# Kernel optimization log

Hardware: AMD Instinct MI355X
Metric: run time of the kernel (lower is better)

## Reference

```python
import jax, jax.numpy as jnp
import numpy as np

S, B, H, D, G = 2048, 2, 16, 128, 16  # seq, batch, heads, head_dim, v-quant groups


def setup_inputs() -> dict:
    key = jax.random.key(0)
    ks = jax.random.split(key, 9)
    # int8-valued activations stored as float (torch code does .to(torch.int8))
    q = jax.random.randint(ks[0], (S, B, H, D), -128, 128).astype(jnp.float32)
    k = jax.random.randint(ks[1], (S, B, H, D), -128, 128).astype(jnp.float32)
    v = jax.random.randint(ks[2], (S, B, H, D), -128, 128).astype(jnp.float32)
    qmin = jax.random.normal(ks[3], (S, B, H, 1), jnp.float32) * 0.01
    qscale = jax.random.uniform(ks[4], (S, B, H, 1), jnp.float32, 0.005, 0.02)
    kmin = jax.random.normal(ks[5], (S, B, H, 1), jnp.float32) * 0.01
    kscale = jax.random.uniform(ks[6], (S, B, H, 1), jnp.float32, 0.005, 0.02)
    vmin = jax.random.normal(ks[7], (G, B, H, D, 1), jnp.float32) * 0.01
    vscale = jax.random.uniform(ks[8], (G, B, H, D, 1), jnp.float32, 0.005, 0.02)
    return {"query_layer": q, "key_layer": k, "value_layer": v,
            "qmin": qmin, "qscale": qscale, "kmin": kmin, "kscale": kscale,
            "vmin": vmin, "vscale": vscale, "causal": 1}


def _attention(query_layer, key_layer, value_layer, qmin, qscale, kmin, kscale, vmin, vscale, causal):
    # s b h d -> b h s d ; emulate .to(torch.int8) (values are already int8-range ints)
    q = jnp.transpose(query_layer, (1, 2, 0, 3))
    k = jnp.transpose(key_layer, (1, 2, 0, 3))
    v = jnp.transpose(value_layer, (1, 2, 0, 3))
    # per-token quant factors: s b h 1 -> b h s 1
    qm = jnp.transpose(qmin[..., 0], (1, 2, 0))[..., None]
    qs = jnp.transpose(qscale[..., 0], (1, 2, 0))[..., None]
    km = jnp.transpose(kmin[..., 0], (1, 2, 0))[..., None]
    ksc = jnp.transpose(kscale[..., 0], (1, 2, 0))[..., None]
    # attnq_qk: dequantize per-token then QK^T
    qd = q * qs + qm
    kd = k * ksc + km
    scores = jnp.einsum('bhsd,bhtd->bhst', qd, kd)
    # softmaxq: scale by 1/sqrt(128), causal mask, softmax, int8 requant of probs
    scores = scores * jnp.float32(1.0 / np.sqrt(128.0))
    s = scores.shape[-1]
    if causal:
        mask = jnp.tril(jnp.ones((s, s), dtype=bool))
        scores = jnp.where(mask, scores, jnp.float32(-1e9))
    probs = jax.nn.softmax(scores, axis=-1)
    pmin = jnp.min(probs, axis=-1, keepdims=True)
    pmax = jnp.max(probs, axis=-1, keepdims=True)
    pscale = (pmax - pmin) / 255.0 + jnp.float32(1e-12)
    quant_prob = jnp.round((probs - pmin) / pscale)  # int8-range prob codes
    # attnq_pv: dequant probs (per query token) and V (per sequence group) then PV
    pd = quant_prob * pscale + pmin
    vm = jnp.transpose(vmin[..., 0], (1, 2, 0, 3))  # b h g d
    vs = jnp.transpose(vscale[..., 0], (1, 2, 0, 3))
    gs = v.shape[2] // vm.shape[2]  # group size along sequence
    vd = v * jnp.repeat(vs, gs, axis=2) + jnp.repeat(vm, gs, axis=2)
    out = jnp.einsum('bhst,bhtd->bhsd', pd, vd)
    b, h, sq, d = out.shape
    return jnp.transpose(out, (2, 0, 1, 3)).reshape(sq, b, h * d)  # s b (h d)


def reference(query_layer, key_layer, value_layer, qmin, qscale, kmin, kscale, vmin, vscale, causal):
    return _attention(query_layer, key_layer, value_layer, qmin, qscale, kmin, kscale, vmin, vscale, causal)
```

## Files before the change

kernel.cpp:

```cpp
#include <hip/hip_runtime.h>
#include <math.h>


#define S_LEN 2048
#define BATCH 2
#define NH    16
#define HD    128
#define RSTR  4096
#define SCALE2 (0.08838834764831845f * 1.4426950408889634f)
#define EXP2F(x) __builtin_amdgcn_exp2f(x)

typedef int v4i __attribute__((ext_vector_type(4)));
#define MFMA16(a,b,c) __builtin_amdgcn_mfma_i32_16x16x64_i8((a),(b),(c),0,0,0)

#define WS_K8   0u
#define WS_V8T  (8u*1024u*1024u)
#define WS_SQ   (16u*1024u*1024u)
#define WS_SK   (WS_SQ + 256u*1024u)
#define WS_GSV  (WS_SK + 256u*1024u)
#define WS_VSUM (WS_GSV + 256u*1024u)

__global__ __launch_bounds__(256) void prep_sums(
    const float* __restrict__ Q, const float* __restrict__ K,
    signed char* __restrict__ K8, float* __restrict__ SQs, float* __restrict__ SKs)
{
    int idx = blockIdx.x*256 + threadIdx.x;
    int tensor = blockIdx.y;
    const float* src = tensor ? K : Q;
    int tau = idx >> 5, dg = idx & 31;
    float4 x = *(const float4*)(src + (size_t)tau*128 + 4*dg);
    float ssum = x.x + x.y + x.z + x.w;
    #pragma unroll
    for (int off = 16; off >= 1; off >>= 1) ssum += __shfl_xor(ssum, off);
    if (tensor) {
        int a=(int)x.x, b2=(int)x.y, c=(int)x.z, d=(int)x.w;
        ((int*)K8)[(size_t)tau*32 + dg] = (a&255)|((b2&255)<<8)|((c&255)<<16)|((d&255)<<24);
        if ((threadIdx.x & 31) == 0) SKs[tau] = ssum;
    } else {
        if ((threadIdx.x & 31) == 0) SQs[tau] = ssum;
    }
}

__device__ __forceinline__ int sbsum(unsigned p) {
    return (int)(signed char)(p) + (int)(signed char)(p>>8)
         + (int)(signed char)(p>>16) + (int)(signed char)(p>>24);
}

__global__ __launch_bounds__(256) void prep_v(
    const float* __restrict__ V, signed char* __restrict__ V8T, float* __restrict__ GSV)
{
    __shared__ int v8i[128*33];
    int tid = threadIdx.x;
    int bh = blockIdx.x & 31, ck = blockIdx.x >> 5;
    int b = bh >> 4, h = bh & 15;
    int t0 = ck * 128;
    int boff = b*2048 + h*128;
    #pragma unroll
    for (int it = 0; it < 16; ++it) {
        int idx = tid + it*256;
        int t = idx >> 5, dw = idx & 31;
        float4 x = *(const float4*)(V + (size_t)(t0+t)*RSTR + boff + 4*dw);
        int a=(int)x.x, b2=(int)x.y, c=(int)x.z, d=(int)x.w;
        v8i[t*33 + dw] = (a&255)|((b2&255)<<8)|((c&255)<<16)|((d&255)<<24);
    }
    __syncthreads();
    #pragma unroll
    for (int it = 0; it < 4; ++it) {
        int j = tid + it*256;
        int tg = j & 31, dw = j >> 5;
        unsigned r0 = (unsigned)v8i[(4*tg+0)*33 + dw];
        unsigned r1 = (unsigned)v8i[(4*tg+1)*33 + dw];
        unsigned r2 = (unsigned)v8i[(4*tg+2)*33 + dw];
        unsigned r3 = (unsigned)v8i[(4*tg+3)*33 + dw];
        unsigned x01 = __builtin_amdgcn_perm(r1, r0, 0x05010400u);
        unsigned x23 = __builtin_amdgcn_perm(r3, r2, 0x05010400u);
        unsigned y01 = __builtin_amdgcn_perm(r1, r0, 0x07030602u);
        unsigned y23 = __builtin_amdgcn_perm(r3, r2, 0x07030602u);
        unsigned p[4];
        p[0] = __builtin_amdgcn_perm(x23, x01, 0x05040100u);
        p[1] = __builtin_amdgcn_perm(x23, x01, 0x07060302u);
        p[2] = __builtin_amdgcn_perm(y23, y01, 0x05040100u);
        p[3] = __builtin_amdgcn_perm(y23, y01, 0x07060302u);
        int s[4];
        #pragma unroll
        for (int jj = 0; jj < 4; ++jj) {
            int d = 4*dw + jj;
            *(int*)(V8T + ((size_t)bh*128 + d)*2048 + t0 + 4*tg) = (int)p[jj];
            s[jj] = sbsum(p[jj]);
        }
        #pragma unroll
        for (int off = 1; off < 32; off <<= 1) {
            #pragma unroll
            for (int jj = 0; jj < 4; ++jj) s[jj] += __shfl_xor(s[jj], off);
        }
        if (tg == 0) {
            #pragma unroll
            for (int jj = 0; jj < 4; ++jj)
                GSV[((size_t)bh*16 + ck)*128 + 4*dw + jj] = (float)s[jj];
        }
    }
}

__global__ __launch_bounds__(256) void prep_vsum(
    const float* __restrict__ GSV, const float* __restrict__ VSC,
    const float* __restrict__ VMN, float* __restrict__ VSUM)
{
    int idx = blockIdx.x*256 + threadIdx.x;
    int bh = idx >> 7, d = idx & 127;
    int b = bh >> 4, h = bh & 15;
    float acc = 0.f;
    for (int g = 0; g < 16; ++g) {
        float gs = GSV[((size_t)bh*16 + g)*128 + d];
        int vi = ((g*BATCH + b)*NH + h)*HD + d;
        acc = fmaf(VSC[vi], gs, fmaf(128.0f, VMN[vi], acc));
    }
    VSUM[bh*128 + d] = acc;
}

__global__ __launch_bounds__(256, 2) void attn_main(
    const float* __restrict__ Q,
    const signed char* __restrict__ K8, const signed char* __restrict__ V8T,
    const float* __restrict__ QMN, const float* __restrict__ QSC,
    const float* __restrict__ KMN, const float* __restrict__ KSC,
    const float* __restrict__ VMN, const float* __restrict__ VSC,
    const float* __restrict__ SQs, const float* __restrict__ SKs,
    const float* __restrict__ GSV, const float* __restrict__ VSUM,
    const int* __restrict__ CAUSAL, float* __restrict__ OUT)
{
    __shared__ __align__(16) signed char q8s[64*144];
    __shared__ __align__(16) signed char k8s[128*144];
    __shared__ __align__(16) signed char v8s[128*144];
    __shared__ __align__(16) signed char pcs[64*144];
    __shared__ float rs_c1[64], rs_c2[64], rs_c3[64];
    __shared__ float rs_mx[64], rs_den[64], rs_mn[64];
    __shared__ float rs_u1[64], rs_w1[64], rs_psc[64], rs_pmn[64];
    __shared__ float ktA[128], ktB[128], ktC[128];
    __shared__ float vsA[128], vsB[128], vsC[128];

    const int tid  = threadIdx.x;
    const int w    = tid >> 6;
    const int lane = tid & 63;
    const int n    = lane & 15;
    const int quad = lane >> 4;
    const int bhi  = blockIdx.x & 31;
    const int qt   = 31 - (int)(blockIdx.x >> 5);
    const int b    = bhi >> 4, h = bhi & 15;
    const int causal = *CAUSAL;
    const int s0   = qt * 64;
    const int boff = b*2048 + h*128;
    const v4i vzero = {0,0,0,0};
    const v4i ones  = {0x01010101,0x01010101,0x01010101,0x01010101};

    #pragma unroll
    for (int it = 0; it < 8; ++it) {
        int idx = tid + it*256;
        int row = idx >> 5, d4 = (idx & 31) << 2;
        float4 x = *(const float4*)(Q + (size_t)(s0+row)*RSTR + boff + d4);
        int a=(int)x.x, b2=(int)x.y, c=(int)x.z, d=(int)x.w;
        *(int*)(q8s + row*144 + d4) = (a&255)|((b2&255)<<8)|((c&255)<<16)|((d&255)<<24);
    }
    if (tid < 64) {
        int si = (s0 + tid)*32 + bhi;
        float qs = QSC[si], qm = QMN[si];
        rs_c1[tid] = qs; rs_c2[tid] = qm;
        rs_c3[tid] = fmaf(qs, SQs[si], 128.0f*qm);
    }
    __syncthreads();

    const int kt_end = causal ? ((s0 + 63) >> 7) : 15;

    float c1r[4], c2r[4], c3r[4]; int qgr[4];
    #pragma unroll
    for (int r = 0; r < 4; ++r) {
        int qq = 16*w + 4*quad + r;
        c1r[r] = rs_c1[qq]; c2r[r] = rs_c2[qq]; c3r[r] = rs_c3[qq];
        qgr[r] = s0 + qq;
    }
    v4i a0p = *(const v4i*)(q8s + (16*w + n)*144 + 16*quad);
    v4i a1p = *(const v4i*)(q8s + (16*w + n)*144 + 64 + 16*quad);

    float m[4], l[4], mn[4];
    #pragma unroll
    for (int r = 0; r < 4; ++r) { m[r] = -INFINITY; l[r] = 0.f; mn[r] = INFINITY; }

#define P1_TILE(MASKED)                                                          \
  do {                                                                           \
    const int t0g = kt * 128;                                                    \
    __syncthreads();                                                             \
    _Pragma("unroll")                                                            \
    for (int it = 0; it < 4; ++it) {                                             \
        int idx = tid + it*256;                                                  \
        int trow = idx >> 3, doff = (idx & 7) << 4;                              \
        *(uint4*)(k8s + trow*144 + doff) =                                       \
            *(const uint4*)(K8 + ((size_t)(t0g+trow)*32 + bhi)*128 + doff);      \
    }                                                                            \
    if (tid < 128) {                                                             \
        int si = (t0g + tid)*32 + bhi;                                           \
        ktA[tid] = KSC[si]*SCALE2; ktB[tid] = KMN[si]*SCALE2; ktC[tid] = SKs[si];\
    }                                                                            \
    __syncthreads();                                                             \
    float tmax[4], sarr[8][4];                                                   \
    _Pragma("unroll")                                                            \
    for (int r = 0; r < 4; ++r) tmax[r] = -INFINITY;                             \
    _Pragma("unroll")                                                            \
    for (int tb = 0; tb < 8; ++tb) {                                             \
        v4i b0 = *(const v4i*)(k8s + (16*tb + n)*144 + 16*quad);                 \
        v4i b1 = *(const v4i*)(k8s + (16*tb + n)*144 + 64 + 16*quad);            \
        v4i acc = MFMA16(a0p, b0, vzero);                                        \
        acc = MFMA16(a1p, b1, acc);                                              \
        int tl = 16*tb + n;                                                      \
        float ks = ktA[tl], km = ktB[tl], sk = ktC[tl];                          \
        _Pragma("unroll")                                                        \
        for (int r = 0; r < 4; ++r) {                                            \
            float Sf = (float)acc[r];                                            \
            float sv = fmaf(ks, fmaf(c1r[r], Sf, c2r[r]*sk), km*c3r[r]);         \
            if (MASKED) sv = (t0g + tl > qgr[r]) ? -INFINITY : sv;               \
            sarr[tb][r] = sv;                                                    \
            tmax[r] = fmaxf(tmax[r], sv);                                        \
            mn[r] = fminf(mn[r], sv);                                            \
        }                                                                        \
    }                                                                            \
    _Pragma("unroll")                                                            \
    for (int r = 0; r < 4; ++r) {                                                \
        float mm = fmaxf(m[r], tmax[r]);                                         \
        if (mm > -INFINITY) {                                                    \
            float a2 = l[r]*EXP2F(m[r]-mm);                                      \
            _Pragma("unroll")                                                    \
            for (int tb = 0; tb < 8; ++tb) a2 += EXP2F(sarr[tb][r]-mm);          \
            l[r] = a2; m[r] = mm;                                                \
        }                                                                        \
    }                                                                            \
  } while (0)

    {
        int kt;
        for (kt = 0; kt < kt_end; ++kt) P1_TILE(false);
        kt = kt_end;
        if (causal) P1_TILE(true); else P1_TILE(false);
    }

    #pragma unroll
    for (int r = 0; r < 4; ++r) {
        #pragma unroll
        for (int off = 1; off < 16; off <<= 1) {
            float m2 = __shfl_xor(m[r], off);
            float l2 = __shfl_xor(l[r], off);
            float n2 = __shfl_xor(mn[r], off);
            float mm = fmaxf(m[r], m2);
            if (mm > -INFINITY) l[r] = l[r]*EXP2F(m[r]-mm) + l2*EXP2F(m2-mm);
            m[r] = mm;
            mn[r] = fminf(mn[r], n2);
        }
        if (n == 0) {
            int qq = 16*w + 4*quad + r;
            rs_mx[qq] = m[r]; rs_den[qq] = l[r]; rs_mn[qq] = mn[r];
        }
    }
    __syncthreads();
    if (tid < 64) {
        float mx = rs_mx[tid], den = rs_den[tid], mnv = rs_mn[tid];
        float invd = 1.0f/den;
        int s = s0 + tid;
        bool hasmask = (causal != 0) && (s < S_LEN-1);
        float pmin = hasmask ? 0.0f : EXP2F(mnv - mx)*invd;
        float psc  = (invd - pmin)/255.0f + 1e-12f;
        float ipsc = 1.0f/psc;
        rs_u1[tid] = invd*ipsc; rs_w1[tid] = -pmin*ipsc;
        rs_psc[tid] = psc; rs_pmn[tid] = pmin;
    }

    float outa[4][8];
    #pragma unroll
    for (int r = 0; r < 4; ++r)
        #pragma unroll
        for (int db = 0; db < 8; ++db) outa[r][db] = 0.f;

#define P2_TILE(MASKED)                                                          \
  do {                                                                           \
    const int t0g = kt * 128;                                                    \
    __syncthreads();                                                             \
    _Pragma("unroll")                                                            \
    for (int it = 0; it < 4; ++it) {                                             \
        int idx = tid + it*256;                                                  \
        int trow = idx >> 3, doff = (idx & 7) << 4;                              \
        *(uint4*)(k8s + trow*144 + doff) =                                       \
            *(const uint4*)(K8 + ((size_t)(t0g+trow)*32 + bhi)*128 + doff);      \
        *(uint4*)(v8s + trow*144 + doff) =                                       \
            *(const uint4*)(V8T + ((size_t)bhi*128 + trow)*2048 + t0g + doff);   \
    }                                                                            \
    if (tid < 128) {                                                             \
        int si = (t0g + tid)*32 + bhi;                                           \
        ktA[tid] = KSC[si]*SCALE2; ktB[tid] = KMN[si]*SCALE2; ktC[tid] = SKs[si];\
    } else {                                                                     \
        int d = tid - 128;                                                       \
        int vi = ((kt*BATCH + b)*NH + h)*HD + d;                                 \
        float vs = VSC[vi], vm = VMN[vi];                                        \
        float gs = GSV[((size_t)bhi*16 + kt)*128 + d];                           \
        vsA[d] = vs; vsB[d] = vm;                                                \
        vsC[d] = fmaf(128.0f*vs, gs, 16384.0f*vm);                               \
    }                                                                            \
    __syncthreads();                                                             \
    _Pragma("unroll")                                                            \
    for (int rb = 0; rb < 2; ++rb) {                                             \
        int trow = 32*w + 16*rb;                                                 \
        v4i a0 = *(const v4i*)(k8s + (trow + n)*144 + 16*quad);                  \
        v4i a1 = *(const v4i*)(k8s + (trow + n)*144 + 64 + 16*quad);             \
        float ksr[4], kmr[4], skr[4];                                            \
        int tgb = t0g + trow + 4*quad;                                           \
        _Pragma("unroll")                                                        \
        for (int r = 0; r < 4; ++r) {                                            \
            int tl = trow + 4*quad + r;                                          \
            ksr[r] = ktA[tl]; kmr[r] = ktB[tl]; skr[r] = ktC[tl];                \
        }                                                                        \
        _Pragma("unroll")                                                        \
        for (int cb = 0; cb < 4; ++cb) {                                         \
            v4i b0 = *(const v4i*)(q8s + (16*cb + n)*144 + 16*quad);             \
            v4i b1 = *(const v4i*)(q8s + (16*cb + n)*144 + 64 + 16*quad);        \
            v4i acc = MFMA16(a0, b0, vzero);                                     \
            acc = MFMA16(a1, b1, acc);                                           \
            int qcol = 16*cb + n, qg = s0 + qcol;                                \
            float c1 = rs_c1[qcol], c2 = rs_c2[qcol], c3 = rs_c3[qcol];          \
            float mxq = rs_mx[qcol], u1 = rs_u1[qcol], w1 = rs_w1[qcol];         \
            int packed = 0;                                                      \
            _Pragma("unroll")                                                    \
            for (int r = 0; r < 4; ++r) {                                        \
                float Sf = (float)acc[r];                                        \
                float x = fmaf(ksr[r], fmaf(c1, Sf, c2*skr[r]),                  \
                               fmaf(kmr[r], c3, -mxq));                          \
                if (MASKED) x = (tgb + r > qg) ? -INFINITY : x;                  \
                float e = EXP2F(x);                                              \
                int ci = (int)rintf(fmaf(e, u1, w1));                            \
                packed |= ci << (8*r);                                           \
            }                                                                    \
            packed ^= 0x80808080;                       \
            *(int*)(pcs + qcol*144 + trow + 4*quad) = packed;                    \
        }                                                                        \
    }                                                                            \
    __syncthreads();                                                             \
    {                                                                            \
        v4i a0 = *(const v4i*)(pcs + (16*w + n)*144 + 16*quad);                  \
        v4i a1 = *(const v4i*)(pcs + (16*w + n)*144 + 64 + 16*quad);             \
        v4i c1a = MFMA16(a0, ones, vzero);                                       \
        c1a = MFMA16(a1, ones, c1a);                                             \
        float c1f[4];                                                            \
        _Pragma("unroll")                                                        \
        for (int r = 0; r < 4; ++r) c1f[r] = (float)c1a[r];                      \
        _Pragma("unroll")                                                        \
        for (int db = 0; db < 8; ++db) {                                         \
            v4i b0 = *(const v4i*)(v8s + (16*db + n)*144 + 16*quad);             \
            v4i b1 = *(const v4i*)(v8s + (16*db + n)*144 + 64 + 16*quad);        \
            v4i cv = MFMA16(a0, b0, vzero);                                      \
            cv = MFMA16(a1, b1, cv);                                             \
            int d = 16*db + n;                                                   \
            float vs = vsA[d], vm = vsB[d], Bd = vsC[d];                         \
            _Pragma("unroll")                                                    \
            for (int r = 0; r < 4; ++r)                                          \
                outa[r][db] = fmaf(vs, (float)cv[r],                             \
                                   fmaf(vm, c1f[r], outa[r][db] + Bd));          \
        }                                                                        \
    }                                                                            \
  } while (0)

    {
        int kt;
        for (kt = 0; kt < kt_end; ++kt) P2_TILE(false);
        kt = kt_end;
        if (causal) P2_TILE(true); else P2_TILE(false);
    }

    float pscr[4], pmnr[4];
    #pragma unroll
    for (int r = 0; r < 4; ++r) {
        int qq = 16*w + 4*quad + r;
        pscr[r] = rs_psc[qq]; pmnr[r] = rs_pmn[qq];
    }
    #pragma unroll
    for (int db = 0; db < 8; ++db) {
        int d = 16*db + n;
        float vsum = VSUM[bhi*128 + d];
        #pragma unroll
        for (int r = 0; r < 4; ++r) {
            int s = s0 + 16*w + 4*quad + r;
            OUT[(size_t)s*RSTR + boff + d] = fmaf(pscr[r], outa[r][db], pmnr[r]*vsum);
        }
    }
}

extern "C" void kernel_launch(void* const* d_in, const int* in_sizes, int n_in,
                              void* d_out, int out_size, void* d_ws, size_t ws_size,
                              hipStream_t stream) {
    (void)in_sizes; (void)n_in; (void)out_size; (void)ws_size;
    const float* Q   = (const float*)d_in[0];
    const float* K   = (const float*)d_in[1];
    const float* V   = (const float*)d_in[2];
    const float* QMN = (const float*)d_in[3];
    const float* QSC = (const float*)d_in[4];
    const float* KMN = (const float*)d_in[5];
    const float* KSC = (const float*)d_in[6];
    const float* VMN = (const float*)d_in[7];
    const float* VSC = (const float*)d_in[8];
    const int*   CS  = (const int*)d_in[9];
    float* out = (float*)d_out;

    char* ws = (char*)d_ws;
    signed char* K8  = (signed char*)(ws + WS_K8);
    signed char* V8T = (signed char*)(ws + WS_V8T);
    float* SQs  = (float*)(ws + WS_SQ);
    float* SKs  = (float*)(ws + WS_SK);
    float* GSVp = (float*)(ws + WS_GSV);
    float* VSUM = (float*)(ws + WS_VSUM);

    prep_sums<<<dim3(8192, 2), 256, 0, stream>>>(Q, K, K8, SQs, SKs);
    prep_v<<<512, 256, 0, stream>>>(V, V8T, GSVp);
    prep_vsum<<<16, 256, 0, stream>>>(GSVp, VSC, VMN, VSUM);
    attn_main<<<1024, 256, 0, stream>>>(Q, K8, V8T, QMN, QSC, KMN, KSC, VMN, VSC,
                                        SQs, SKs, GSVp, VSUM, CS, out);
}
```

Baseline: 263.9 us.

## Prefetch next K/V tiles into registers and merge prep kernels

```diff
diff --git a/kernel.cpp b/kernel.cpp
--- a/kernel.cpp
+++ b/kernel.cpp
@@ -19,100 +19,105 @@
 #define WS_SK   (WS_SQ + 256u*1024u)
 #define WS_GSV  (WS_SK + 256u*1024u)
 #define WS_VSUM (WS_GSV + 256u*1024u)
-
-__global__ __launch_bounds__(256) void prep_sums(
-    const float* __restrict__ Q, const float* __restrict__ K,
-    signed char* __restrict__ K8, float* __restrict__ SQs, float* __restrict__ SKs)
-{
-    int idx = blockIdx.x*256 + threadIdx.x;
-    int tensor = blockIdx.y;
-    const float* src = tensor ? K : Q;
-    int tau = idx >> 5, dg = idx & 31;
-    float4 x = *(const float4*)(src + (size_t)tau*128 + 4*dg);
-    float ssum = x.x + x.y + x.z + x.w;
-    #pragma unroll
-    for (int off = 16; off >= 1; off >>= 1) ssum += __shfl_xor(ssum, off);
-    if (tensor) {
-        int a=(int)x.x, b2=(int)x.y, c=(int)x.z, d=(int)x.w;
-        ((int*)K8)[(size_t)tau*32 + dg] = (a&255)|((b2&255)<<8)|((c&255)<<16)|((d&255)<<24);
-        if ((threadIdx.x & 31) == 0) SKs[tau] = ssum;
-    } else {
-        if ((threadIdx.x & 31) == 0) SQs[tau] = ssum;
-    }
-}
+#define WS_CGS  (WS_VSUM + 64u*1024u)
 
 __device__ __forceinline__ int sbsum(unsigned p) {
     return (int)(signed char)(p) + (int)(signed char)(p>>8)
          + (int)(signed char)(p>>16) + (int)(signed char)(p>>24);
 }
 
-__global__ __launch_bounds__(256) void prep_v(
-    const float* __restrict__ V, signed char* __restrict__ V8T, float* __restrict__ GSV)
+__global__ __launch_bounds__(256) void prep_pack(
+    const float* __restrict__ Q, const float* __restrict__ K, const float* __restrict__ V,
+    signed char* __restrict__ K8, float* __restrict__ SQs, float* __restrict__ SKs,
+    signed char* __restrict__ V8T, float* __restrict__ GSV)
 {
     __shared__ int v8i[128*33];
-    int tid = threadIdx.x;
-    int bh = blockIdx.x & 31, ck = blockIdx.x >> 5;
-    int b = bh >> 4, h = bh & 15;
-    int t0 = ck * 128;
-    int boff = b*2048 + h*128;
-    #pragma unroll
-    for (int it = 0; it < 16; ++it) {
-        int idx = tid + it*256;
-        int t = idx >> 5, dw = idx & 31;
-        float4 x = *(const float4*)(V + (size_t)(t0+t)*RSTR + boff + 4*dw);
-        int a=(int)x.x, b2=(int)x.y, c=(int)x.z, d=(int)x.w;
-        v8i[t*33 + dw] = (a&255)|((b2&255)<<8)|((c&255)<<16)|((d&255)<<24);
-    }
-    __syncthreads();
-    #pragma unroll
-    for (int it = 0; it < 4; ++it) {
-        int j = tid + it*256;
-        int tg = j & 31, dw = j >> 5;
-        unsigned r0 = (unsigned)v8i[(4*tg+0)*33 + dw];
-        unsigned r1 = (unsigned)v8i[(4*tg+1)*33 + dw];
-        unsigned r2 = (unsigned)v8i[(4*tg+2)*33 + dw];
-        unsigned r3 = (unsigned)v8i[(4*tg+3)*33 + dw];
-        unsigned x01 = __builtin_amdgcn_perm(r1, r0, 0x05010400u);
-        unsigned x23 = __builtin_amdgcn_perm(r3, r2, 0x05010400u);
-        unsigned y01 = __builtin_amdgcn_perm(r1, r0, 0x07030602u);
-        unsigned y23 = __builtin_amdgcn_perm(r3, r2, 0x07030602u);
-        unsigned p[4];
-        p[0] = __builtin_amdgcn_perm(x23, x01, 0x05040100u);
-        p[1] = __builtin_amdgcn_perm(x23, x01, 0x07060302u);
-        p[2] = __builtin_amdgcn_perm(y23, y01, 0x05040100u);
-        p[3] = __builtin_amdgcn_perm(y23, y01, 0x07060302u);
-        int s[4];
-        #pragma unroll
-        for (int jj = 0; jj < 4; ++jj) {
-            int d = 4*dw + jj;
-            *(int*)(V8T + ((size_t)bh*128 + d)*2048 + t0 + 4*tg) = (int)p[jj];
-            s[jj] = sbsum(p[jj]);
-        }
-        #pragma unroll
-        for (int off = 1; off < 32; off <<= 1) {
+    const int tid = threadIdx.x;
+    const int bx  = blockIdx.x;
+    if (bx < 16384) {
+        const int tensor = bx >> 13;
+        const int idx = (bx & 8191)*256 + tid;
+        const float* src = tensor ? K : Q;
+        int tau = idx >> 5, dg = idx & 31;
+        float4 x = *(const float4*)(src + (size_t)tau*128 + 4*dg);
+        float ssum = x.x + x.y + x.z + x.w;
+        #pragma unroll
+        for (int off = 16; off >= 1; off >>= 1) ssum += __shfl_xor(ssum, off);
+        if (tensor) {
+            int a=(int)x.x, b2=(int)x.y, c=(int)x.z, d=(int)x.w;
+            ((int*)K8)[(size_t)tau*32 + dg] = (a&255)|((b2&255)<<8)|((c&255)<<16)|((d&255)<<24);
+            if ((tid & 31) == 0) SKs[tau] = ssum;
+        } else {
+            if ((tid & 31) == 0) SQs[tau] = ssum;
+        }
+    } else {
+        const int bid = bx - 16384;
+        const int bh = bid & 31, ck = bid >> 5;
+        const int b = bh >> 4, h = bh & 15;
+        const int t0 = ck * 128;
+        const int boff = b*2048 + h*128;
+        #pragma unroll
+        for (int it = 0; it < 16; ++it) {
+            int idx = tid + it*256;
+            int t = idx >> 5, dw = idx & 31;
+            float4 x = *(const float4*)(V + (size_t)(t0+t)*RSTR + boff + 4*dw);
+            int a=(int)x.x, b2=(int)x.y, c=(int)x.z, d=(int)x.w;
+            v8i[t*33 + dw] = (a&255)|((b2&255)<<8)|((c&255)<<16)|((d&255)<<24);
+        }
+        __syncthreads();
+        #pragma unroll
+        for (int it = 0; it < 4; ++it) {
+            int j = tid + it*256;
+            int tg = j & 31, dw = j >> 5;
+            unsigned r0 = (unsigned)v8i[(4*tg+0)*33 + dw];
+            unsigned r1 = (unsigned)v8i[(4*tg+1)*33 + dw];
+            unsigned r2 = (unsigned)v8i[(4*tg+2)*33 + dw];
+            unsigned r3 = (unsigned)v8i[(4*tg+3)*33 + dw];
+            unsigned x01 = __builtin_amdgcn_perm(r1, r0, 0x05010400u);
+            unsigned x23 = __builtin_amdgcn_perm(r3, r2, 0x05010400u);
+            unsigned y01 = __builtin_amdgcn_perm(r1, r0, 0x07030602u);
+            unsigned y23 = __builtin_amdgcn_perm(r3, r2, 0x07030602u);
+            unsigned p[4];
+            p[0] = __builtin_amdgcn_perm(x23, x01, 0x05040100u);
+            p[1] = __builtin_amdgcn_perm(x23, x01, 0x07060302u);
+            p[2] = __builtin_amdgcn_perm(y23, y01, 0x05040100u);
+            p[3] = __builtin_amdgcn_perm(y23, y01, 0x07060302u);
+            int s[4];
             #pragma unroll
-            for (int jj = 0; jj < 4; ++jj) s[jj] += __shfl_xor(s[jj], off);
-        }
-        if (tg == 0) {
+            for (int jj = 0; jj < 4; ++jj) {
+                int d = 4*dw + jj;
+                *(int*)(V8T + ((size_t)bh*128 + d)*2048 + t0 + 4*tg) = (int)p[jj];
+                s[jj] = sbsum(p[jj]);
+            }
             #pragma unroll
-            for (int jj = 0; jj < 4; ++jj)
-                GSV[((size_t)bh*16 + ck)*128 + 4*dw + jj] = (float)s[jj];
+            for (int off = 1; off < 32; off <<= 1) {
+                #pragma unroll
+                for (int jj = 0; jj < 4; ++jj) s[jj] += __shfl_xor(s[jj], off);
+            }
+            if (tg == 0) {
+                #pragma unroll
+                for (int jj = 0; jj < 4; ++jj)
+                    GSV[((size_t)bh*16 + ck)*128 + 4*dw + jj] = (float)s[jj];
+            }
         }
     }
 }
 
 __global__ __launch_bounds__(256) void prep_vsum(
     const float* __restrict__ GSV, const float* __restrict__ VSC,
-    const float* __restrict__ VMN, float* __restrict__ VSUM)
+    const float* __restrict__ VMN, float* __restrict__ VSUM, float* __restrict__ CGS)
 {
     int idx = blockIdx.x*256 + threadIdx.x;
     int bh = idx >> 7, d = idx & 127;
     int b = bh >> 4, h = bh & 15;
-    float acc = 0.f;
+    float acc = 0.f, accb = 0.f;
     for (int g = 0; g < 16; ++g) {
         float gs = GSV[((size_t)bh*16 + g)*128 + d];
         int vi = ((g*BATCH + b)*NH + h)*HD + d;
-        acc = fmaf(VSC[vi], gs, fmaf(128.0f, VMN[vi], acc));
+        float vs = VSC[vi], vm = VMN[vi];
+        acc  = fmaf(vs, gs, fmaf(128.0f, vm, acc));
+        accb = fmaf(128.0f*vs, gs, fmaf(16384.0f, vm, accb));
+        CGS[((size_t)bh*16 + g)*128 + d] = accb;
     }
     VSUM[bh*128 + d] = acc;
 }
@@ -125,6 +130,7 @@
     const float* __restrict__ VMN, const float* __restrict__ VSC,
     const float* __restrict__ SQs, const float* __restrict__ SKs,
     const float* __restrict__ GSV, const float* __restrict__ VSUM,
+    const float* __restrict__ CGS,
     const int* __restrict__ CAUSAL, float* __restrict__ OUT)
 {
     __shared__ __align__(16) signed char q8s[64*144];
@@ -135,7 +141,7 @@
     __shared__ float rs_mx[64], rs_den[64], rs_mn[64];
     __shared__ float rs_u1[64], rs_w1[64], rs_psc[64], rs_pmn[64];
     __shared__ float ktA[128], ktB[128], ktC[128];
-    __shared__ float vsA[128], vsB[128], vsC[128];
+    __shared__ float vsA[128], vsB[128];
 
     const int tid  = threadIdx.x;
     const int w    = tid >> 6;
@@ -165,9 +171,21 @@
         rs_c1[tid] = qs; rs_c2[tid] = qm;
         rs_c3[tid] = fmaf(qs, SQs[si], 128.0f*qm);
     }
+
+    const int kt_end = causal ? ((s0 + 63) >> 7) : 15;
+
+    #pragma unroll
+    for (int it = 0; it < 4; ++it) {
+        int idx = tid + it*256;
+        int trow = idx >> 3, doff = (idx & 7) << 4;
+        *(uint4*)(k8s + trow*144 + doff) =
+            *(const uint4*)(K8 + ((size_t)trow*32 + bhi)*128 + doff);
+    }
+    if (tid < 128) {
+        int si = tid*32 + bhi;
+        ktA[tid] = KSC[si]*SCALE2; ktB[tid] = KMN[si]*SCALE2; ktC[tid] = SKs[si];
+    }
     __syncthreads();
-
-    const int kt_end = causal ? ((s0 + 63) >> 7) : 15;
 
     float c1r[4], c2r[4], c3r[4]; int qgr[4];
     #pragma unroll
@@ -183,22 +201,8 @@
     #pragma unroll
     for (int r = 0; r < 4; ++r) { m[r] = -INFINITY; l[r] = 0.f; mn[r] = INFINITY; }
 
-#define P1_TILE(MASKED)                                                          \
+#define P1_COMPUTE(MASKED, T0G)                                                  \
   do {                                                                           \
-    const int t0g = kt * 128;                                                    \
-    __syncthreads();                                                             \
-    _Pragma("unroll")                                                            \
-    for (int it = 0; it < 4; ++it) {                                             \
-        int idx = tid + it*256;                                                  \
-        int trow = idx >> 3, doff = (idx & 7) << 4;                              \
-        *(uint4*)(k8s + trow*144 + doff) =                                       \
-            *(const uint4*)(K8 + ((size_t)(t0g+trow)*32 + bhi)*128 + doff);      \
-    }                                                                            \
-    if (tid < 128) {                                                             \
-        int si = (t0g + tid)*32 + bhi;                                           \
-        ktA[tid] = KSC[si]*SCALE2; ktB[tid] = KMN[si]*SCALE2; ktC[tid] = SKs[si];\
-    }                                                                            \
-    __syncthreads();                                                             \
     float tmax[4], sarr[8][4];                                                   \
     _Pragma("unroll")                                                            \
     for (int r = 0; r < 4; ++r) tmax[r] = -INFINITY;                             \
@@ -209,12 +213,12 @@
         v4i acc = MFMA16(a0p, b0, vzero);                                        \
         acc = MFMA16(a1p, b1, acc);                                              \
         int tl = 16*tb + n;                                                      \
-        float ks = ktA[tl], km = ktB[tl], sk = ktC[tl];                          \
+        float kA = ktA[tl], kB = ktB[tl], kC = ktC[tl];                          \
         _Pragma("unroll")                                                        \
         for (int r = 0; r < 4; ++r) {                                            \
             float Sf = (float)acc[r];                                            \
-            float sv = fmaf(ks, fmaf(c1r[r], Sf, c2r[r]*sk), km*c3r[r]);         \
-            if (MASKED) sv = (t0g + tl > qgr[r]) ? -INFINITY : sv;               \
+            float sv = fmaf(kA, fmaf(c1r[r], Sf, c2r[r]*kC), kB*c3r[r]);         \
+            if (MASKED) sv = ((T0G) + tl > qgr[r]) ? -INFINITY : sv;             \
             sarr[tb][r] = sv;                                                    \
             tmax[r] = fmaxf(tmax[r], sv);                                        \
             mn[r] = fminf(mn[r], sv);                                            \
@@ -224,19 +228,45 @@
     for (int r = 0; r < 4; ++r) {                                                \
         float mm = fmaxf(m[r], tmax[r]);                                         \
         if (mm > -INFINITY) {                                                    \
-            float a2 = l[r]*EXP2F(m[r]-mm);                                      \
-            _Pragma("unroll")                                                    \
-            for (int tb = 0; tb < 8; ++tb) a2 += EXP2F(sarr[tb][r]-mm);          \
-            l[r] = a2; m[r] = mm;                                                \
+            float e0 = EXP2F(sarr[0][r]-mm) + EXP2F(sarr[1][r]-mm);              \
+            float e1 = EXP2F(sarr[2][r]-mm) + EXP2F(sarr[3][r]-mm);              \
+            float e2 = EXP2F(sarr[4][r]-mm) + EXP2F(sarr[5][r]-mm);              \
+            float e3 = EXP2F(sarr[6][r]-mm) + EXP2F(sarr[7][r]-mm);              \
+            l[r] = fmaf(l[r], EXP2F(m[r]-mm), (e0+e1)+(e2+e3));                  \
+            m[r] = mm;                                                           \
         }                                                                        \
     }                                                                            \
   } while (0)
 
-    {
-        int kt;
-        for (kt = 0; kt < kt_end; ++kt) P1_TILE(false);
-        kt = kt_end;
-        if (causal) P1_TILE(true); else P1_TILE(false);
+    for (int kt = 0; ; ++kt) {
+        const int t0g = kt * 128;
+        const bool has_next = kt < kt_end;
+        uint4 pk[4]; float nA = 0.f, nB = 0.f, nC = 0.f;
+        if (has_next) {
+            const int t0n = t0g + 128;
+            #pragma unroll
+            for (int it = 0; it < 4; ++it) {
+                int idx = tid + it*256;
+                int trow = idx >> 3, doff = (idx & 7) << 4;
+                pk[it] = *(const uint4*)(K8 + ((size_t)(t0n+trow)*32 + bhi)*128 + doff);
+            }
+            if (tid < 128) {
+                int si = (t0n + tid)*32 + bhi;
+                nA = KSC[si]; nB = KMN[si]; nC = SKs[si];
+            }
+        }
+        if (causal && kt == kt_end) P1_COMPUTE(true, t0g);
+        else                        P1_COMPUTE(false, t0g);
+        if (!has_next) break;
+        __syncthreads();
+        #pragma unroll
+        for (int it = 0; it < 4; ++it) {
+            int idx = tid + it*256;
+            int trow = idx >> 3, doff = (idx & 7) << 4;
+            *(uint4*)(k8s + trow*144 + doff) = pk[it];
+        }
+        if (tid < 128) { ktA[tid] = nA*SCALE2; ktB[tid] = nB*SCALE2; ktC[tid] = nC; }
+        __syncthreads();
     }
 
     #pragma unroll
@@ -269,44 +299,40 @@
         rs_psc[tid] = psc; rs_pmn[tid] = pmin;
     }
 
+    #pragma unroll
+    for (int it = 0; it < 4; ++it) {
+        int idx = tid + it*256;
+        int trow = idx >> 3, doff = (idx & 7) << 4;
+        *(uint4*)(k8s + trow*144 + doff) =
+            *(const uint4*)(K8 + ((size_t)trow*32 + bhi)*128 + doff);
+        *(uint4*)(v8s + trow*144 + doff) =
+            *(const uint4*)(V8T + ((size_t)bhi*128 + trow)*2048 + doff);
+    }
+    if (tid < 128) {
+        int si = tid*32 + bhi;
+        ktA[tid] = KSC[si]*SCALE2; ktB[tid] = KMN[si]*SCALE2; ktC[tid] = SKs[si];
+    } else {
+        int d = tid - 128;
+        int vi = (b*NH + h)*HD + d;
+        vsA[d] = VSC[vi]; vsB[d] = VMN[vi];
+    }
+    __syncthreads();
+
     float outa[4][8];
     #pragma unroll
     for (int r = 0; r < 4; ++r)
         #pragma unroll
         for (int db = 0; db < 8; ++db) outa[r][db] = 0.f;
 
-#define P2_TILE(MASKED)                                                          \
+#define P2_COMPUTE(MASKED, T0G)                                                  \
   do {                                                                           \
-    const int t0g = kt * 128;                                                    \
-    __syncthreads();                                                             \
-    _Pragma("unroll")                                                            \
-    for (int it = 0; it < 4; ++it) {                                             \
-        int idx = tid + it*256;                                                  \
-        int trow = idx >> 3, doff = (idx & 7) << 4;                              \
-        *(uint4*)(k8s + trow*144 + doff) =                                       \
-            *(const uint4*)(K8 + ((size_t)(t0g+trow)*32 + bhi)*128 + doff);      \
-        *(uint4*)(v8s + trow*144 + doff) =                                       \
-            *(const uint4*)(V8T + ((size_t)bhi*128 + trow)*2048 + t0g + doff);   \
-    }                                                                            \
-    if (tid < 128) {                                                             \
-        int si = (t0g + tid)*32 + bhi;                                           \
-        ktA[tid] = KSC[si]*SCALE2; ktB[tid] = KMN[si]*SCALE2; ktC[tid] = SKs[si];\
-    } else {                                                                     \
-        int d = tid - 128;                                                       \
-        int vi = ((kt*BATCH + b)*NH + h)*HD + d;                                 \
-        float vs = VSC[vi], vm = VMN[vi];                                        \
-        float gs = GSV[((size_t)bhi*16 + kt)*128 + d];                           \
-        vsA[d] = vs; vsB[d] = vm;                                                \
-        vsC[d] = fmaf(128.0f*vs, gs, 16384.0f*vm);                               \
-    }                                                                            \
-    __syncthreads();                                                             \
     _Pragma("unroll")                                                            \
     for (int rb = 0; rb < 2; ++rb) {                                             \
         int trow = 32*w + 16*rb;                                                 \
         v4i a0 = *(const v4i*)(k8s + (trow + n)*144 + 16*quad);                  \
         v4i a1 = *(const v4i*)(k8s + (trow + n)*144 + 64 + 16*quad);             \
         float ksr[4], kmr[4], skr[4];                                            \
-        int tgb = t0g + trow + 4*quad;                                           \
+        int tgb = (T0G) + trow + 4*quad;                                         \
         _Pragma("unroll")                                                        \
         for (int r = 0; r < 4; ++r) {                                            \
             int tl = trow + 4*quad + r;                                          \
@@ -352,20 +378,51 @@
             v4i cv = MFMA16(a0, b0, vzero);                                      \
             cv = MFMA16(a1, b1, cv);                                             \
             int d = 16*db + n;                                                   \
-            float vs = vsA[d], vm = vsB[d], Bd = vsC[d];                         \
+            float vs = vsA[d], vm = vsB[d];                                      \
             _Pragma("unroll")                                                    \
             for (int r = 0; r < 4; ++r)                                          \
                 outa[r][db] = fmaf(vs, (float)cv[r],                             \
-                                   fmaf(vm, c1f[r], outa[r][db] + Bd));          \
+                                   fmaf(vm, c1f[r], outa[r][db]));               \
         }                                                                        \
     }                                                                            \
   } while (0)
 
-    {
-        int kt;
-        for (kt = 0; kt < kt_end; ++kt) P2_TILE(false);
-        kt = kt_end;
-        if (causal) P2_TILE(true); else P2_TILE(false);
+    for (int kt = 0; ; ++kt) {
+        const int t0g = kt * 128;
+        const bool has_next = kt < kt_end;
+        uint4 pk[4], pv[4]; float nA = 0.f, nB = 0.f, nC = 0.f;
+        if (has_next) {
+            const int t0n = t0g + 128;
+            #pragma unroll
+            for (int it = 0; it < 4; ++it) {
+                int idx = tid + it*256;
+                int trow = idx >> 3, doff = (idx & 7) << 4;
+                pk[it] = *(const uint4*)(K8 + ((size_t)(t0n+trow)*32 + bhi)*128 + doff);
+                pv[it] = *(const uint4*)(V8T + ((size_t)bhi*128 + trow)*2048 + t0n + doff);
+            }
+            if (tid < 128) {
+                int si = (t0n + tid)*32 + bhi;
+                nA = KSC[si]; nB = KMN[si]; nC = SKs[si];
+            } else {
+                int d = tid - 128;
+                int vi = (((kt+1)*BATCH + b)*NH + h)*HD + d;
+                nA = VSC[vi]; nB = VMN[vi];
+            }
+        }
+        if (causal && kt == kt_end) P2_COMPUTE(true, t0g);
+        else                        P2_COMPUTE(false, t0g);
+        if (!has_next) break;
+        __syncthreads();
+        #pragma unroll
+        for (int it = 0; it < 4; ++it) {
+            int idx = tid + it*256;
+            int trow = idx >> 3, doff = (idx & 7) << 4;
+            *(uint4*)(k8s + trow*144 + doff) = pk[it];
+            *(uint4*)(v8s + trow*144 + doff) = pv[it];
+        }
+        if (tid < 128) { ktA[tid] = nA*SCALE2; ktB[tid] = nB*SCALE2; ktC[tid] = nC; }
+        else           { int d = tid - 128; vsA[d] = nA; vsB[d] = nB; }
+        __syncthreads();
     }
 
     float pscr[4], pmnr[4];
@@ -378,10 +435,11 @@
     for (int db = 0; db < 8; ++db) {
         int d = 16*db + n;
         float vsum = VSUM[bhi*128 + d];
+        float cgs  = CGS[((size_t)bhi*16 + kt_end)*128 + d];
         #pragma unroll
         for (int r = 0; r < 4; ++r) {
             int s = s0 + 16*w + 4*quad + r;
-            OUT[(size_t)s*RSTR + boff + d] = fmaf(pscr[r], outa[r][db], pmnr[r]*vsum);
+            OUT[(size_t)s*RSTR + boff + d] = fmaf(pscr[r], outa[r][db] + cgs, pmnr[r]*vsum);
         }
     }
 }
@@ -409,10 +467,10 @@
     float* SKs  = (float*)(ws + WS_SK);
     float* GSVp = (float*)(ws + WS_GSV);
     float* VSUM = (float*)(ws + WS_VSUM);
-
-    prep_sums<<<dim3(8192, 2), 256, 0, stream>>>(Q, K, K8, SQs, SKs);
-    prep_v<<<512, 256, 0, stream>>>(V, V8T, GSVp);
-    prep_vsum<<<16, 256, 0, stream>>>(GSVp, VSC, VMN, VSUM);
+    float* CGSp = (float*)(ws + WS_CGS);
+
+    prep_pack<<<16384 + 512, 256, 0, stream>>>(Q, K, V, K8, SQs, SKs, V8T, GSVp);
+    prep_vsum<<<16, 256, 0, stream>>>(GSVp, VSC, VMN, VSUM, CGSp);
     attn_main<<<1024, 256, 0, stream>>>(Q, K8, V8T, QMN, QSC, KMN, KSC, VMN, VSC,
-                                        SQs, SKs, GSVp, VSUM, CS, out);
+                                        SQs, SKs, GSVp, VSUM, CGSp, CS, out);
 }
```

Measured after the change: 327.5 us. 24.1% more time.
